# Kernel optimization log

Measured on AMD Instinct MI355X. Metric: run time of the kernel, lower is better.

The kernel has to match this reference:

```python
import jax, jax.numpy as jnp
import numpy as np

NS = 10000   # servers
ND = 50000   # devices
H = 512      # hidden dim
E = 300000   # edges per relation
L = 4        # total SAGEConv layers (input + 2 hidden + output)


def segment_mean(vals, seg, num_segments):
    # scatter-mean aggregation (PyG 'mean' aggr); empty segments -> 0
    s = jax.ops.segment_sum(vals, seg, num_segments=num_segments)
    cnt = jax.ops.segment_sum(jnp.ones((seg.shape[0], 1), vals.dtype), seg,
                              num_segments=num_segments)
    return s / jnp.maximum(cnt, 1.0)


def setup_inputs() -> dict:
    key = jax.random.key(0)
    ks = jax.random.split(key, 12)
    scale = 0.05
    return {
        "x_servers": jax.random.normal(ks[0], (NS, 64), jnp.float32),
        "x_devices": jax.random.normal(ks[1], (ND, 32), jnp.float32),
        "W_srv": jax.random.normal(ks[2], (64, H), jnp.float32) * scale,
        "b_srv": jnp.zeros((H,), jnp.float32),
        "W_dev": jax.random.normal(ks[3], (32, H), jnp.float32) * scale,
        "b_dev": jnp.zeros((H,), jnp.float32),
        # rel 0: servers->devices (updates devices); rel 1: devices->servers
        "Wl": jax.random.normal(ks[4], (L, 2, H, H), jnp.float32) * scale,
        "bl": jnp.zeros((L, 2, H), jnp.float32),
        "Wr": jax.random.normal(ks[5], (L, 2, H, H), jnp.float32) * scale,
        "e_sd_src": jax.random.randint(ks[6], (E,), 0, NS, jnp.int32),
        "e_sd_dst": jax.random.randint(ks[7], (E,), 0, ND, jnp.int32),
        "e_ds_src": jax.random.randint(ks[8], (E,), 0, ND, jnp.int32),
        "e_ds_dst": jax.random.randint(ks[9], (E,), 0, NS, jnp.int32),
    }


def reference(x_servers, x_devices, W_srv, b_srv, W_dev, b_dev,
              Wl, bl, Wr, e_sd_src, e_sd_dst, e_ds_src, e_ds_dst):
    # per-type input projection (no activation, as in GNN.forward)
    hs = x_servers @ W_srv + b_srv   # [NS, H]
    hd = x_devices @ W_dev + b_dev   # [ND, H]
    for l in range(L):
        # gather source features per edge, scatter-mean to destination
        agg_d = segment_mean(hs[e_sd_src], e_sd_dst, ND)  # servers -> devices
        agg_s = segment_mean(hd[e_ds_src], e_ds_dst, NS)  # devices -> servers
        # SAGEConv: lin_l(agg) + lin_r(x_dst), then relu
        new_d = jax.nn.relu(agg_d @ Wl[l, 0] + bl[l, 0] + hd @ Wr[l, 0])
        new_s = jax.nn.relu(agg_s @ Wl[l, 1] + bl[l, 1] + hs @ Wr[l, 1])
        hs, hd = new_s, new_d
    return (hs, hd)
```

## Files before the change

kernel.cpp:

```cpp
#include <hip/hip_runtime.h>
#include <cstdint>

#define NSRV 10000
#define NDEV 50000
#define HDIM 512
#define NEDGE 300000
#define NLAY 4
#define SCHUNK 2048
#define NCH_D ((NDEV + SCHUNK - 1) / SCHUNK)
#define NCH_S ((NSRV + SCHUNK - 1) / SCHUNK)

typedef unsigned int u32;
typedef unsigned short u16;

typedef __bf16 bf16x8 __attribute__((ext_vector_type(8)));
typedef float f32x4 __attribute__((ext_vector_type(4)));

__device__ __forceinline__ float bflo(u32 u) { return __uint_as_float(u << 16); }
__device__ __forceinline__ float bfhi(u32 u) { return __uint_as_float(u & 0xffff0000u); }
__device__ __forceinline__ float bf2f(u16 v) { return __uint_as_float((u32)v << 16); }
__device__ __forceinline__ u16 f2bf(float f) {
    u32 u = __float_as_uint(f);
    u += 0x7fffu + ((u >> 16) & 1u);
    return (u16)(u >> 16);
}
__device__ __forceinline__ u32 pack2(float a, float b) {
    return (u32)f2bf(a) | ((u32)f2bf(b) << 16);
}

__global__ void cast_bf16(const float* __restrict__ src, u16* __restrict__ dst, int n2) {
    int i = blockIdx.x * 256 + threadIdx.x;
    if (i < n2) {
        float2 v = *(const float2*)(src + 2 * (size_t)i);
        *(u32*)(dst + 2 * (size_t)i) = pack2(v.x, v.y);
    }
}

__global__ void transpose_w(const float* __restrict__ Wl, const float* __restrict__ Wr,
                            u16* __restrict__ WlT, u16* __restrict__ WrT) {
    __shared__ float t[32][33];
    int z = blockIdx.z;
    const float* Wsrc = ((z < 8) ? Wl : Wr) + (size_t)(z & 7) * HDIM * HDIM;
    u16* Wdst = ((z < 8) ? WlT : WrT) + (size_t)(z & 7) * HDIM * HDIM;
    int n0 = blockIdx.x * 32, k0 = blockIdx.y * 32;
    int x = threadIdx.x, y = threadIdx.y;
#pragma unroll
    for (int i = 0; i < 4; ++i)
        t[y + 8 * i][x] = Wsrc[(size_t)(k0 + y + 8 * i) * HDIM + n0 + x];
    __syncthreads();
    if (x < 16) {
#pragma unroll
        for (int i = 0; i < 4; ++i) {
            int n = n0 + y + 8 * i;
            u32 v = pack2(t[2 * x][y + 8 * i], t[2 * x + 1][y + 8 * i]);
            *(u32*)(Wdst + (size_t)n * HDIM + k0 + 2 * x) = v;
        }
    }
}

template <int K>
__global__ void transpose_wp(const float* __restrict__ W, u16* __restrict__ WT) {
    __shared__ float t[32][33];
    int n0 = blockIdx.x * 32, k0 = blockIdx.y * 32;
    int x = threadIdx.x, y = threadIdx.y;
#pragma unroll
    for (int i = 0; i < 4; ++i)
        t[y + 8 * i][x] = W[(size_t)(k0 + y + 8 * i) * HDIM + n0 + x];
    __syncthreads();
    if (x < 16) {
#pragma unroll
        for (int i = 0; i < 4; ++i) {
            int n = n0 + y + 8 * i;
            u32 v = pack2(t[2 * x][y + 8 * i], t[2 * x + 1][y + 8 * i]);
            *(u32*)(WT + (size_t)n * K + k0 + 2 * x) = v;
        }
    }
}

template <int KTOT>
__launch_bounds__(256, 2)
__global__ void proj_gemm(const u16* __restrict__ A, const u16* __restrict__ B,
                          const float* __restrict__ bias, u16* __restrict__ C, int M) {
    constexpr int NKC = KTOT / 8;
    __shared__ __align__(16) u16 As[NKC][128][8];
    __shared__ __align__(16) u16 Bs[NKC][128][8];
    const int tid = threadIdx.x;
    const int lane = tid & 63;
    const int w = tid >> 6;
    const int m0 = blockIdx.x * 128, n0 = blockIdx.y * 128;
    const int wm = w >> 1, wn = w & 1;
    const int g = lane >> 4, r = lane & 15;

    for (int idx = tid; idx < NKC * 128; idx += 256) {
        int row = idx / NKC, kc = idx % NKC;
        int ra = m0 + row; if (ra > M - 1) ra = M - 1;
        *(uint4*)&As[kc][row][0] = *(const uint4*)(A + (size_t)ra * KTOT + kc * 8);
        *(uint4*)&Bs[kc][row][0] = *(const uint4*)(B + (size_t)(n0 + row) * KTOT + kc * 8);
    }
    __syncthreads();

    f32x4 acc[4][4];
#pragma unroll
    for (int i = 0; i < 4; ++i)
#pragma unroll
        for (int j = 0; j < 4; ++j) acc[i][j] = (f32x4){0.f, 0.f, 0.f, 0.f};

#pragma unroll
    for (int t = 0; t < KTOT / 32; ++t) {
        bf16x8 af[4], bfr[4];
#pragma unroll
        for (int i = 0; i < 4; ++i) {
            af[i]  = *(const bf16x8*)&As[t * 4 + g][wm * 64 + i * 16 + r][0];
            bfr[i] = *(const bf16x8*)&Bs[t * 4 + g][wn * 64 + i * 16 + r][0];
        }
#pragma unroll
        for (int i = 0; i < 4; ++i)
#pragma unroll
            for (int j = 0; j < 4; ++j)
                acc[i][j] = __builtin_amdgcn_mfma_f32_16x16x32_bf16(af[i], bfr[j], acc[i][j], 0, 0, 0);
    }
    __syncthreads();

    float bv[4];
#pragma unroll
    for (int j = 0; j < 4; ++j) bv[j] = bias[n0 + wn * 64 + j * 16 + r];

    u16* ep = ((u16*)As) + w * 1024;
    const int rr = lane >> 3;
    const int cc = (lane & 7) * 8;
#pragma unroll
    for (int i = 0; i < 4; ++i) {
#pragma unroll
        for (int j = 0; j < 4; ++j)
#pragma unroll
            for (int q = 0; q < 4; ++q)
                ep[(g * 4 + q) * 64 + j * 16 + r] = f2bf(acc[i][j][q] + bv[j]);
        __syncthreads();
        int row0 = m0 + wm * 64 + i * 16 + rr;
        int row1 = row0 + 8;
        uint4 v0 = *(uint4*)&ep[rr * 64 + cc];
        uint4 v1 = *(uint4*)&ep[(rr + 8) * 64 + cc];
        if (row0 < M) *(uint4*)(C + (size_t)row0 * HDIM + n0 + wn * 64 + cc) = v0;
        if (row1 < M) *(uint4*)(C + (size_t)row1 * HDIM + n0 + wn * 64 + cc) = v1;
        __syncthreads();
    }
}

__global__ void count_k(const int* __restrict__ d_sd, const int* __restrict__ d_ds,
                        int* __restrict__ cd, int* __restrict__ cs) {
    int i = blockIdx.x * 256 + threadIdx.x;
    if (i < NEDGE) atomicAdd(&cd[d_sd[i]], 1);
    else if (i < 2 * NEDGE) atomicAdd(&cs[d_ds[i - NEDGE]], 1);
}

__global__ void scan_a_both(const int* __restrict__ cd, int* __restrict__ od, int* __restrict__ csd,
                            const int* __restrict__ cs, int* __restrict__ os, int* __restrict__ css) {
    __shared__ int wsum[4];
    int blk = blockIdx.x;
    const int* c; int* o; int* csum; int n; int cb;
    if (blk < NCH_D) { c = cd; o = od; csum = csd; n = NDEV; cb = blk; }
    else             { c = cs; o = os; csum = css; n = NSRV; cb = blk - NCH_D; }
    int tid = threadIdx.x;
    int base = cb * SCHUNK;
    int idx0 = base + tid * 8;
    int v[8];
    int s = 0;
#pragma unroll
    for (int i = 0; i < 8; ++i) {
        int idx = idx0 + i;
        v[i] = (idx < n) ? c[idx] : 0;
        s += v[i];
    }
    int lane = tid & 63, wv = tid >> 6;
    int ss = s;
#pragma unroll
    for (int off = 1; off < 64; off <<= 1) {
        int t = __shfl_up(ss, off);
        if (lane >= off) ss += t;
    }
    if (lane == 63) wsum[wv] = ss;
    __syncthreads();
    int woff = 0;
#pragma unroll
    for (int i = 0; i < 4; ++i)
        if (i < wv) woff += wsum[i];
    int ex = woff + ss - s;
#pragma unroll
    for (int i = 0; i < 8; ++i) {
        int idx = idx0 + i;
        if (idx < n) o[idx] = ex;
        ex += v[i];
    }
    if (tid == 255) csum[cb] = woff + ss;
}

__global__ void scan_k(const int* __restrict__ cA, int* __restrict__ oA, int* __restrict__ uA, int nA,
                       const int* __restrict__ cB, int* __restrict__ oB, int* __restrict__ uB, int nB) {
    const int* c; int* o; int* u; int n;
    if (blockIdx.x == 0) { c = cA; o = oA; u = uA; n = nA; }
    else                 { c = cB; o = oB; u = uB; n = nB; }
    int lane = threadIdx.x;
    int carry = 0;
    for (int base = 0; base < n; base += 64) {
        int idx = base + lane;
        int v = (idx < n) ? c[idx] : 0;
        int s = v;
#pragma unroll
        for (int off = 1; off < 64; off <<= 1) {
            int t = __shfl_up(s, off);
            if (lane >= off) s += t;
        }
        if (idx < n) { int ex = carry + s - v; o[idx] = ex; u[idx] = ex; }
        carry += __shfl(s, 63);
    }
}

__global__ void scan_c_both(int* __restrict__ od, int* __restrict__ curd, const int* __restrict__ csxd,
                            int* __restrict__ os, int* __restrict__ curs, const int* __restrict__ csxs) {
    int i = blockIdx.x * 256 + threadIdx.x;
    if (i < NDEV) {
        int v = od[i] + csxd[i / SCHUNK];
        od[i] = v;
        curd[i] = v;
    } else if (i < NDEV + NSRV) {
        int j = i - NDEV;
        int v = os[j] + csxs[j / SCHUNK];
        os[j] = v;
        curs[j] = v;
    }
}

__global__ void fill_k(const int* __restrict__ s_sd, const int* __restrict__ d_sd,
                       int* __restrict__ cur_d, int* __restrict__ srcs_d,
                       const int* __restrict__ s_ds, const int* __restrict__ d_ds,
                       int* __restrict__ cur_s, int* __restrict__ srcs_s) {
    int i = blockIdx.x * 256 + threadIdx.x;
    if (i < NEDGE) {
        int p = atomicAdd(&cur_d[d_sd[i]], 1);
        srcs_d[p] = s_sd[i];
    } else if (i < 2 * NEDGE) {
        int j = i - NEDGE;
        int p = atomicAdd(&cur_s[d_ds[j]], 1);
        srcs_s[p] = s_ds[j];
    }
}

__global__ void aggregate_both(const u16* __restrict__ hs, const u16* __restrict__ hd,
                               const int* __restrict__ offs_d, const int* __restrict__ cnt_d,
                               const int* __restrict__ src_d,
                               const int* __restrict__ offs_s, const int* __restrict__ cnt_s,
                               const int* __restrict__ src_s,
                               u16* __restrict__ agg_d, u16* __restrict__ agg_s) {
    int wv = threadIdx.x >> 6, lane = threadIdx.x & 63;
    int d = blockIdx.x * 4 + wv;
    const u16* h; const int* offs; const int* cnt; const int* srcs; u16* agg; int idx;
    if (d < NDEV)              { h = hs; offs = offs_d; cnt = cnt_d; srcs = src_d; agg = agg_d; idx = d; }
    else if (d < NDEV + NSRV)  { h = hd; offs = offs_s; cnt = cnt_s; srcs = src_s; agg = agg_s; idx = d - NDEV; }
    else return;
    int beg = offs[idx], deg = cnt[idx];
    float acc[8] = {0.f, 0.f, 0.f, 0.f, 0.f, 0.f, 0.f, 0.f};
    const size_t lanecol = (size_t)lane * 8;
    auto accum = [&](const uint4& q) {
        acc[0] += bflo(q.x); acc[1] += bfhi(q.x);
        acc[2] += bflo(q.y); acc[3] += bfhi(q.y);
        acc[4] += bflo(q.z); acc[5] += bfhi(q.z);
        acc[6] += bflo(q.w); acc[7] += bfhi(q.w);
    };
    for (int t0 = 0; t0 < deg; t0 += 64) {
        int nch = min(64, deg - t0);
        int sv = (t0 + lane < deg) ? srcs[beg + t0 + lane] : 0;
        int j = 0;
        for (; j + 8 <= nch; j += 8) {
            uint4 q[8];
#pragma unroll
            for (int u_ = 0; u_ < 8; ++u_) {
                int s = __shfl(sv, j + u_);
                q[u_] = *(const uint4*)(h + (size_t)s * HDIM + lanecol);
            }
#pragma unroll
            for (int u_ = 0; u_ < 8; ++u_) accum(q[u_]);
        }
        for (; j + 4 <= nch; j += 4) {
            uint4 q[4];
#pragma unroll
            for (int u_ = 0; u_ < 4; ++u_) {
                int s = __shfl(sv, j + u_);
                q[u_] = *(const uint4*)(h + (size_t)s * HDIM + lanecol);
            }
#pragma unroll
            for (int u_ = 0; u_ < 4; ++u_) accum(q[u_]);
        }
        for (; j < nch; ++j) {
            int s = __shfl(sv, j);
            const uint4 q = *(const uint4*)(h + (size_t)s * HDIM + lanecol);
            accum(q);
        }
    }
    float sc = 1.f / (float)(deg > 0 ? deg : 1);
    uint4 o;
    o.x = pack2(acc[0] * sc, acc[1] * sc);
    o.y = pack2(acc[2] * sc, acc[3] * sc);
    o.z = pack2(acc[4] * sc, acc[5] * sc);
    o.w = pack2(acc[6] * sc, acc[7] * sc);
    *(uint4*)(agg + (size_t)idx * HDIM + lanecol) = o;
}

__launch_bounds__(512, 2)
__global__ void gemm_both(const u16* __restrict__ A1d, const u16* __restrict__ A2d,
                          const u16* __restrict__ B1d, const u16* __restrict__ B2d,
                          const float* __restrict__ bd, u16* __restrict__ Cd, int Md, int MBd, int GD,
                          const u16* __restrict__ A1s, const u16* __restrict__ A2s,
                          const u16* __restrict__ B1s, const u16* __restrict__ B2s,
                          const float* __restrict__ bs, u16* __restrict__ Cs, int Ms, int MBs) {
    int b = blockIdx.x;
    const u16 *A1, *A2, *B1, *B2; const float* bias; u16* C; int M, MB;
    if (b < GD) { A1 = A1d; A2 = A2d; B1 = B1d; B2 = B2d; bias = bd; C = Cd; M = Md; MB = MBd; }
    else { b -= GD; A1 = A1s; A2 = A2s; B1 = B1s; B2 = B2s; bias = bs; C = Cs; M = Ms; MB = MBs; }
    const int mi = (b >> 5) * 8 + (b & 7);
    const int ni = (b >> 3) & 3;
    if (mi >= MB) return;

    __shared__ __align__(16) u16 As[2][4][256][8];
    __shared__ __align__(16) u16 Bs[2][4][128][8];
    const int tid = threadIdx.x;
    const int lane = tid & 63;
    const int w = tid >> 6;
    const int m0 = mi * 256, n0 = ni * 128;
    const int wm = w >> 1, wn = w & 1;
    const int g = lane >> 4, r = lane & 15;

    const int srow = tid >> 2;
    const int skc  = tid & 3;

    f32x4 acc[4][4];
#pragma unroll
    for (int i = 0; i < 4; ++i)
#pragma unroll
        for (int j = 0; j < 4; ++j) acc[i][j] = (f32x4){0.f, 0.f, 0.f, 0.f};

    uint4 ra0, ra1, rb0;
    auto gload = [&](int kt) {
        const u16* Ap = (kt < 16) ? A1 : A2;
        const u16* Bp = (kt < 16) ? B1 : B2;
        const int kb = (kt & 15) * 32 + skc * 8;
        int r0 = m0 + srow;       if (r0 > M - 1) r0 = M - 1;
        int r1 = m0 + srow + 128; if (r1 > M - 1) r1 = M - 1;
        ra0 = *(const uint4*)(Ap + (size_t)r0 * HDIM + kb);
        ra1 = *(const uint4*)(Ap + (size_t)r1 * HDIM + kb);
        rb0 = *(const uint4*)(Bp + (size_t)(n0 + srow) * HDIM + kb);
    };
    auto swrite = [&](int buf) {
        *(uint4*)&As[buf][skc][srow][0]       = ra0;
        *(uint4*)&As[buf][skc][srow + 128][0] = ra1;
        *(uint4*)&Bs[buf][skc][srow][0]       = rb0;
    };
    auto compute = [&](int buf) {
        bf16x8 af[4], bfr[4];
#pragma unroll
        for (int i = 0; i < 4; ++i) {
            af[i]  = *(const bf16x8*)&As[buf][g][wm * 64 + i * 16 + r][0];
            bfr[i] = *(const bf16x8*)&Bs[buf][g][wn * 64 + i * 16 + r][0];
        }
#pragma unroll
        for (int i = 0; i < 4; ++i)
#pragma unroll
            for (int j = 0; j < 4; ++j)
                acc[i][j] = __builtin_amdgcn_mfma_f32_16x16x32_bf16(af[i], bfr[j], acc[i][j], 0, 0, 0);
    };

    gload(0);
    swrite(0);
    __syncthreads();
    for (int kt = 0; kt < 32; ++kt) {
        if (kt < 31) gload(kt + 1);
        compute(kt & 1);
        if (kt < 31) swrite((kt + 1) & 1);
        __syncthreads();
    }

    float bv[4];
#pragma unroll
    for (int j = 0; j < 4; ++j) bv[j] = bias[n0 + wn * 64 + j * 16 + r];

    u16* ep = ((u16*)As) + w * 2048;
    const int rr = lane >> 3;
    const int cc = (lane & 7) * 8;
#pragma unroll
    for (int ih = 0; ih < 2; ++ih) {
#pragma unroll
        for (int ii = 0; ii < 2; ++ii) {
            int i = ih * 2 + ii;
#pragma unroll
            for (int j = 0; j < 4; ++j)
#pragma unroll
                for (int q = 0; q < 4; ++q)
                    ep[ii * 1024 + (g * 4 + q) * 64 + j * 16 + r] =
                        f2bf(fmaxf(acc[i][j][q] + bv[j], 0.f));
        }
        __syncthreads();
#pragma unroll
        for (int ii = 0; ii < 2; ++ii) {
            int i = ih * 2 + ii;
            int row0 = m0 + wm * 64 + i * 16 + rr;
            int row1 = row0 + 8;
            uint4 v0 = *(uint4*)&ep[ii * 1024 + rr * 64 + cc];
            uint4 v1 = *(uint4*)&ep[ii * 1024 + (rr + 8) * 64 + cc];
            if (row0 < M) *(uint4*)(C + (size_t)row0 * HDIM + n0 + wn * 64 + cc) = v0;
            if (row1 < M) *(uint4*)(C + (size_t)row1 * HDIM + n0 + wn * 64 + cc) = v1;
        }
        __syncthreads();
    }
}

__global__ void expand_k(float* out, int lo, int hi) {
    const u16* src = (const u16*)out;
    int j = lo + blockIdx.x * 256 + threadIdx.x;
    if (j < hi) {
        float v = bf2f(src[j]);
        out[(size_t)j] = v;
    }
}
__global__ void expand_final(float* out, int n) {
    __shared__ u16 tmp[4096];
    const u16* src = (const u16*)out;
    int tid = threadIdx.x;
    for (int i = tid; i < n; i += blockDim.x) tmp[i] = src[i];
    __syncthreads();
    for (int i = tid; i < n; i += blockDim.x) out[(size_t)i] = bf2f(tmp[i]);
}

extern "C" void kernel_launch(void* const* d_in, const int* in_sizes, int n_in,
                              void* d_out, int out_size, void* d_ws, size_t ws_size,
                              hipStream_t stream) {
    const float* x_s   = (const float*)d_in[0];
    const float* x_d   = (const float*)d_in[1];
    const float* W_srv = (const float*)d_in[2];
    const float* b_srv = (const float*)d_in[3];
    const float* W_dev = (const float*)d_in[4];
    const float* b_dev = (const float*)d_in[5];
    const float* Wl    = (const float*)d_in[6];
    const float* bl    = (const float*)d_in[7];
    const float* Wr    = (const float*)d_in[8];
    const int* e_sd_src = (const int*)d_in[9];
    const int* e_sd_dst = (const int*)d_in[10];
    const int* e_ds_src = (const int*)d_in[11];
    const int* e_ds_dst = (const int*)d_in[12];

    const size_t NTOT = (size_t)(NSRV + NDEV) * HDIM;
    float* fout = (float*)d_out;
    u16* u = (u16*)d_out;
    u16* hA_s = u;
    u16* hA_d = u + (size_t)NSRV * HDIM;
    u16* hB_s = u + NTOT;
    u16* hB_d = u + NTOT + (size_t)NSRV * HDIM;

    char* p = (char*)d_ws;
    auto carve = [&](size_t bytes) -> void* {
        void* ret = (void*)p;
        p += (bytes + 255) & ~(size_t)255;
        return ret;
    };
    int* cnt_d = (int*)carve((size_t)NDEV * 4);
    int* cnt_s = (int*)carve((size_t)NSRV * 4);
    int* off_d = (int*)carve((size_t)NDEV * 4);
    int* off_s = (int*)carve((size_t)NSRV * 4);
    int* cur_d = (int*)carve((size_t)NDEV * 4);
    int* cur_s = (int*)carve((size_t)NSRV * 4);
    int* src_d = (int*)carve((size_t)NEDGE * 4);
    int* src_s = (int*)carve((size_t)NEDGE * 4);
    int* csum_d = (int*)carve(64 * 4);
    int* csum_s = (int*)carve(64 * 4);
    int* csx_d  = (int*)carve(64 * 4);
    int* csx_s  = (int*)carve(64 * 4);
    u16* WlT   = (u16*)carve((size_t)NLAY * 2 * HDIM * HDIM * 2);
    u16* WrT   = (u16*)carve((size_t)NLAY * 2 * HDIM * HDIM * 2);
    u16* agg_d = (u16*)carve((size_t)NDEV * HDIM * 2);
    u16* agg_s = (u16*)carve((size_t)NSRV * HDIM * 2);
    u16* xb_s  = (u16*)carve((size_t)NSRV * 64 * 2);
    u16* xb_d  = (u16*)carve((size_t)NDEV * 32 * 2);
    u16* WTp_s = (u16*)carve((size_t)HDIM * 64 * 2);
    u16* WTp_d = (u16*)carve((size_t)HDIM * 32 * 2);

    hipMemsetAsync(cnt_d, 0, (size_t)NDEV * 4, stream);
    hipMemsetAsync(cnt_s, 0, (size_t)NSRV * 4, stream);

    cast_bf16<<<(NSRV * 64 / 2 + 255) / 256, 256, 0, stream>>>(x_s, xb_s, NSRV * 64 / 2);
    cast_bf16<<<(NDEV * 32 / 2 + 255) / 256, 256, 0, stream>>>(x_d, xb_d, NDEV * 32 / 2);
    transpose_wp<64><<<dim3(16, 2), dim3(32, 8), 0, stream>>>(W_srv, WTp_s);
    transpose_wp<32><<<dim3(16, 1), dim3(32, 8), 0, stream>>>(W_dev, WTp_d);
    transpose_w<<<dim3(16, 16, 16), dim3(32, 8), 0, stream>>>(Wl, Wr, WlT, WrT);

    proj_gemm<64><<<dim3((NSRV + 127) / 128, 4), 256, 0, stream>>>(xb_s, WTp_s, b_srv, hA_s, NSRV);
    proj_gemm<32><<<dim3((NDEV + 127) / 128, 4), 256, 0, stream>>>(xb_d, WTp_d, b_dev, hA_d, NDEV);

    count_k<<<(2 * NEDGE + 255) / 256, 256, 0, stream>>>(e_sd_dst, e_ds_dst, cnt_d, cnt_s);
    scan_a_both<<<NCH_D + NCH_S, 256, 0, stream>>>(cnt_d, off_d, csum_d, cnt_s, off_s, csum_s);
    scan_k<<<2, 64, 0, stream>>>(csum_d, csx_d, csx_d, NCH_D, csum_s, csx_s, csx_s, NCH_S);
    scan_c_both<<<(NDEV + NSRV + 255) / 256, 256, 0, stream>>>(off_d, cur_d, csx_d, off_s, cur_s, csx_s);
    fill_k<<<(2 * NEDGE + 255) / 256, 256, 0, stream>>>(e_sd_src, e_sd_dst, cur_d, src_d,
                                                        e_ds_src, e_ds_dst, cur_s, src_s);

    const int MB_D = (NDEV + 255) / 256;
    const int MB_S = (NSRV + 255) / 256;
    const int GD = ((MB_D + 7) / 8) * 32;
    const int GS = ((MB_S + 7) / 8) * 32;

    for (int l = 0; l < NLAY; ++l) {
        const u16* hs_in = (l & 1) ? hB_s : hA_s;
        const u16* hd_in = (l & 1) ? hB_d : hA_d;
        u16* hs_out = (l & 1) ? hA_s : hB_s;
        u16* hd_out = (l & 1) ? hA_d : hB_d;

        const u16* WlT0 = WlT + (size_t)(l * 2 + 0) * HDIM * HDIM;
        const u16* WrT0 = WrT + (size_t)(l * 2 + 0) * HDIM * HDIM;
        const u16* WlT1 = WlT + (size_t)(l * 2 + 1) * HDIM * HDIM;
        const u16* WrT1 = WrT + (size_t)(l * 2 + 1) * HDIM * HDIM;
        const float* bl0 = bl + (size_t)(l * 2 + 0) * HDIM;
        const float* bl1 = bl + (size_t)(l * 2 + 1) * HDIM;

        aggregate_both<<<(NDEV + NSRV + 3) / 4, 256, 0, stream>>>(
            hs_in, hd_in, off_d, cnt_d, src_d, off_s, cnt_s, src_s, agg_d, agg_s);
        gemm_both<<<GD + GS, 512, 0, stream>>>(
            agg_d, hd_in, WlT0, WrT0, bl0, hd_out, NDEV, MB_D, GD,
            agg_s, hs_in, WlT1, WrT1, bl1, hs_out, NSRV, MB_S);
    }

    int hi = (int)NTOT;
    while (hi > 4000 && (hi % 2 == 0)) {
        int lo = hi / 2;
        int nblk = (hi - lo + 255) / 256;
        expand_k<<<nblk, 256, 0, stream>>>(fout, lo, hi);
        hi = lo;
    }
    expand_final<<<1, 512, 0, stream>>>(fout, hi);
}
```

Measured before the change: 857.1 us.

## Project server features before aggregation to shrink device-side GEMM

Uses linearity of mean aggregation: server features are multiplied by Wl on the 10k server rows first, then gathered and averaged into device rows. The device GEMM then only computes the Wr half (K=512 instead of 1024) and adds the pre-projected aggregate plus ReLU in the epilogue. This cuts device-side GEMM FLOPs roughly in half at the cost of one small extra GEMM and an extra read of agg in the epilogue. Rounding order changes because the projection is rounded to bf16 before averaging.

```diff
diff --git a/kernel.cpp b/kernel.cpp
--- a/kernel.cpp
+++ b/kernel.cpp
@@ -26,6 +26,12 @@
 }
 __device__ __forceinline__ u32 pack2(float a, float b) {
     return (u32)f2bf(a) | ((u32)f2bf(b) << 16);
+}
+__device__ __forceinline__ u32 relu2(u32 v) {
+    return pack2(fmaxf(bflo(v), 0.f), fmaxf(bfhi(v), 0.f));
+}
+__device__ __forceinline__ u32 addrelu2(u32 v, u32 a) {
+    return pack2(fmaxf(bflo(v) + bflo(a), 0.f), fmaxf(bfhi(v) + bfhi(a), 0.f));
 }
 
 __global__ void cast_bf16(const float* __restrict__ src, u16* __restrict__ dst, int n2) {
@@ -146,6 +152,93 @@
     }
 }
 
+__launch_bounds__(256, 2)
+__global__ void gemm_plain(const u16* __restrict__ A, const u16* __restrict__ B,
+                           u16* __restrict__ C, int M, int MB) {
+    const int b = blockIdx.x;
+    const int mi = (b >> 5) * 8 + (b & 7);
+    const int ni = (b >> 3) & 3;
+    if (mi >= MB) return;
+
+    __shared__ __align__(16) u16 As[2][4][128][8];
+    __shared__ __align__(16) u16 Bs[2][4][128][8];
+    const int tid = threadIdx.x;
+    const int lane = tid & 63;
+    const int w = tid >> 6;
+    const int m0 = mi * 128, n0 = ni * 128;
+    const int wm = w >> 1, wn = w & 1;
+    const int g = lane >> 4, r = lane & 15;
+
+    const int srow = tid >> 2;
+    const int skc  = tid & 3;
+
+    f32x4 acc[4][4];
+#pragma unroll
+    for (int i = 0; i < 4; ++i)
+#pragma unroll
+        for (int j = 0; j < 4; ++j) acc[i][j] = (f32x4){0.f, 0.f, 0.f, 0.f};
+
+    uint4 ra0, ra1, rb0, rb1;
+    auto gload = [&](int kt) {
+        const int kb = kt * 32 + skc * 8;
+        int r0 = m0 + srow;      if (r0 > M - 1) r0 = M - 1;
+        int r1 = m0 + srow + 64; if (r1 > M - 1) r1 = M - 1;
+        ra0 = *(const uint4*)(A + (size_t)r0 * HDIM + kb);
+        ra1 = *(const uint4*)(A + (size_t)r1 * HDIM + kb);
+        rb0 = *(const uint4*)(B + (size_t)(n0 + srow) * HDIM + kb);
+        rb1 = *(const uint4*)(B + (size_t)(n0 + srow + 64) * HDIM + kb);
+    };
+    auto swrite = [&](int buf) {
+        *(uint4*)&As[buf][skc][srow][0]      = ra0;
+        *(uint4*)&As[buf][skc][srow + 64][0] = ra1;
+        *(uint4*)&Bs[buf][skc][srow][0]      = rb0;
+        *(uint4*)&Bs[buf][skc][srow + 64][0] = rb1;
+    };
+    auto compute = [&](int buf) {
+        bf16x8 af[4], bfr[4];
+#pragma unroll
+        for (int i = 0; i < 4; ++i) {
+            af[i]  = *(const bf16x8*)&As[buf][g][wm * 64 + i * 16 + r][0];
+            bfr[i] = *(const bf16x8*)&Bs[buf][g][wn * 64 + i * 16 + r][0];
+        }
+#pragma unroll
+        for (int i = 0; i < 4; ++i)
+#pragma unroll
+            for (int j = 0; j < 4; ++j)
+                acc[i][j] = __builtin_amdgcn_mfma_f32_16x16x32_bf16(af[i], bfr[j], acc[i][j], 0, 0, 0);
+    };
+
+    gload(0);
+    swrite(0);
+    __syncthreads();
+    for (int kt = 0; kt < 16; ++kt) {
+        if (kt < 15) gload(kt + 1);
+        compute(kt & 1);
+        if (kt < 15) swrite((kt + 1) & 1);
+        __syncthreads();
+    }
+
+    u16* ep = ((u16*)As) + w * 1024;
+    const int rr = lane >> 3;
+    const int cc = (lane & 7) * 8;
+#pragma unroll
+    for (int i = 0; i < 4; ++i) {
+#pragma unroll
+        for (int j = 0; j < 4; ++j)
+#pragma unroll
+            for (int q = 0; q < 4; ++q)
+                ep[(g * 4 + q) * 64 + j * 16 + r] = f2bf(acc[i][j][q]);
+        __syncthreads();
+        int row0 = m0 + wm * 64 + i * 16 + rr;
+        int row1 = row0 + 8;
+        uint4 v0 = *(uint4*)&ep[rr * 64 + cc];
+        uint4 v1 = *(uint4*)&ep[(rr + 8) * 64 + cc];
+        if (row0 < M) *(uint4*)(C + (size_t)row0 * HDIM + n0 + wn * 64 + cc) = v0;
+        if (row1 < M) *(uint4*)(C + (size_t)row1 * HDIM + n0 + wn * 64 + cc) = v1;
+        __syncthreads();
+    }
+}
+
 __global__ void count_k(const int* __restrict__ d_sd, const int* __restrict__ d_ds,
                         int* __restrict__ cd, int* __restrict__ cs) {
     int i = blockIdx.x * 256 + threadIdx.x;
@@ -245,7 +338,7 @@
     }
 }
 
-__global__ void aggregate_both(const u16* __restrict__ hs, const u16* __restrict__ hd,
+__global__ void aggregate_both(const u16* __restrict__ ps, const u16* __restrict__ hd,
                                const int* __restrict__ offs_d, const int* __restrict__ cnt_d,
                                const int* __restrict__ src_d,
                                const int* __restrict__ offs_s, const int* __restrict__ cnt_s,
@@ -254,7 +347,7 @@
     int wv = threadIdx.x >> 6, lane = threadIdx.x & 63;
     int d = blockIdx.x * 4 + wv;
     const u16* h; const int* offs; const int* cnt; const int* srcs; u16* agg; int idx;
-    if (d < NDEV)              { h = hs; offs = offs_d; cnt = cnt_d; srcs = src_d; agg = agg_d; idx = d; }
+    if (d < NDEV)              { h = ps; offs = offs_d; cnt = cnt_d; srcs = src_d; agg = agg_d; idx = d; }
     else if (d < NDEV + NSRV)  { h = hd; offs = offs_s; cnt = cnt_s; srcs = src_s; agg = agg_s; idx = d - NDEV; }
     else return;
     int beg = offs[idx], deg = cnt[idx];
@@ -308,14 +401,21 @@
 __launch_bounds__(512, 2)
 __global__ void gemm_both(const u16* __restrict__ A1d, const u16* __restrict__ A2d,
                           const u16* __restrict__ B1d, const u16* __restrict__ B2d,
-                          const float* __restrict__ bd, u16* __restrict__ Cd, int Md, int MBd, int GD,
+                          const u16* __restrict__ AGGd, const float* __restrict__ bd,
+                          u16* __restrict__ Cd, int Md, int MBd, int GD,
                           const u16* __restrict__ A1s, const u16* __restrict__ A2s,
                           const u16* __restrict__ B1s, const u16* __restrict__ B2s,
                           const float* __restrict__ bs, u16* __restrict__ Cs, int Ms, int MBs) {
     int b = blockIdx.x;
-    const u16 *A1, *A2, *B1, *B2; const float* bias; u16* C; int M, MB;
-    if (b < GD) { A1 = A1d; A2 = A2d; B1 = B1d; B2 = B2d; bias = bd; C = Cd; M = Md; MB = MBd; }
-    else { b -= GD; A1 = A1s; A2 = A2s; B1 = B1s; B2 = B2s; bias = bs; C = Cs; M = Ms; MB = MBs; }
+    const u16 *A1, *A2, *B1, *B2, *AGG; const float* bias; u16* C; int M, MB, kt0;
+    if (b < GD) {
+        A1 = A1d; A2 = A2d; B1 = B1d; B2 = B2d; AGG = AGGd;
+        bias = bd; C = Cd; M = Md; MB = MBd; kt0 = 16;
+    } else {
+        b -= GD;
+        A1 = A1s; A2 = A2s; B1 = B1s; B2 = B2s; AGG = nullptr;
+        bias = bs; C = Cs; M = Ms; MB = MBs; kt0 = 0;
+    }
     const int mi = (b >> 5) * 8 + (b & 7);
     const int ni = (b >> 3) & 3;
     if (mi >= MB) return;
@@ -368,10 +468,10 @@
                 acc[i][j] = __builtin_amdgcn_mfma_f32_16x16x32_bf16(af[i], bfr[j], acc[i][j], 0, 0, 0);
     };
 
-    gload(0);
+    gload(kt0);
     swrite(0);
     __syncthreads();
-    for (int kt = 0; kt < 32; ++kt) {
+    for (int kt = kt0; kt < 32; ++kt) {
         if (kt < 31) gload(kt + 1);
         compute(kt & 1);
         if (kt < 31) swrite((kt + 1) & 1);
@@ -395,7 +495,7 @@
 #pragma unroll
                 for (int q = 0; q < 4; ++q)
                     ep[ii * 1024 + (g * 4 + q) * 64 + j * 16 + r] =
-                        f2bf(fmaxf(acc[i][j][q] + bv[j], 0.f));
+                        f2bf(acc[i][j][q] + bv[j]);
         }
         __syncthreads();
 #pragma unroll
@@ -405,8 +505,32 @@
             int row1 = row0 + 8;
             uint4 v0 = *(uint4*)&ep[ii * 1024 + rr * 64 + cc];
             uint4 v1 = *(uint4*)&ep[ii * 1024 + (rr + 8) * 64 + cc];
-            if (row0 < M) *(uint4*)(C + (size_t)row0 * HDIM + n0 + wn * 64 + cc) = v0;
-            if (row1 < M) *(uint4*)(C + (size_t)row1 * HDIM + n0 + wn * 64 + cc) = v1;
+            size_t c0 = (size_t)row0 * HDIM + n0 + wn * 64 + cc;
+            size_t c1 = (size_t)row1 * HDIM + n0 + wn * 64 + cc;
+            if (row0 < M) {
+                uint4 o;
+                if (AGG) {
+                    uint4 a = *(const uint4*)(AGG + c0);
+                    o.x = addrelu2(v0.x, a.x); o.y = addrelu2(v0.y, a.y);
+                    o.z = addrelu2(v0.z, a.z); o.w = addrelu2(v0.w, a.w);
+                } else {
+                    o.x = relu2(v0.x); o.y = relu2(v0.y);
+                    o.z = relu2(v0.z); o.w = relu2(v0.w);
+                }
+                *(uint4*)(C + c0) = o;
+            }
+            if (row1 < M) {
+                uint4 o;
+                if (AGG) {
+                    uint4 a = *(const uint4*)(AGG + c1);
+                    o.x = addrelu2(v1.x, a.x); o.y = addrelu2(v1.y, a.y);
+                    o.z = addrelu2(v1.z, a.z); o.w = addrelu2(v1.w, a.w);
+                } else {
+                    o.x = relu2(v1.x); o.y = relu2(v1.y);
+                    o.z = relu2(v1.z); o.w = relu2(v1.w);
+                }
+                *(uint4*)(C + c1) = o;
+            }
         }
         __syncthreads();
     }
@@ -476,6 +600,7 @@
     u16* WrT   = (u16*)carve((size_t)NLAY * 2 * HDIM * HDIM * 2);
     u16* agg_d = (u16*)carve((size_t)NDEV * HDIM * 2);
     u16* agg_s = (u16*)carve((size_t)NSRV * HDIM * 2);
+    u16* ps    = (u16*)carve((size_t)NSRV * HDIM * 2);
     u16* xb_s  = (u16*)carve((size_t)NSRV * 64 * 2);
     u16* xb_d  = (u16*)carve((size_t)NDEV * 32 * 2);
     u16* WTp_s = (u16*)carve((size_t)HDIM * 64 * 2);
@@ -504,6 +629,8 @@
     const int MB_S = (NSRV + 255) / 256;
     const int GD = ((MB_D + 7) / 8) * 32;
     const int GS = ((MB_S + 7) / 8) * 32;
+    const int MB_P = (NSRV + 127) / 128;
+    const int GP = ((MB_P + 7) / 8) * 32;
 
     for (int l = 0; l < NLAY; ++l) {
         const u16* hs_in = (l & 1) ? hB_s : hA_s;
@@ -518,10 +645,11 @@
         const float* bl0 = bl + (size_t)(l * 2 + 0) * HDIM;
         const float* bl1 = bl + (size_t)(l * 2 + 1) * HDIM;
 
+        gemm_plain<<<GP, 256, 0, stream>>>(hs_in, WlT0, ps, NSRV, MB_P);
         aggregate_both<<<(NDEV + NSRV + 3) / 4, 256, 0, stream>>>(
-            hs_in, hd_in, off_d, cnt_d, src_d, off_s, cnt_s, src_s, agg_d, agg_s);
+            ps, hd_in, off_d, cnt_d, src_d, off_s, cnt_s, src_s, agg_d, agg_s);
         gemm_both<<<GD + GS, 512, 0, stream>>>(
-            agg_d, hd_in, WlT0, WrT0, bl0, hd_out, NDEV, MB_D, GD,
+            hd_in, hd_in, WrT0, WrT0, agg_d, bl0, hd_out, NDEV, MB_D, GD,
             agg_s, hs_in, WlT1, WrT1, bl1, hs_out, NSRV, MB_S);
     }
 
```

Result: faster. 837.1 us (-2.3%).
